# Performance work log

Hardware: AMD Instinct MI355X
Metric: run time of the kernel (lower is better)

## Reference

```python
import jax, jax.numpy as jnp
import numpy as np
import math

B, HW, EMBED, HEADS, WS = 32, 56, 192, 6, 7
SHIFT = WS // 2
HD = EMBED // HEADS
NW = HW // WS
NEG = -1e9  # stands in for -inf in the original; avoids NaN-safe issues while masking fully


def _shift_masks():
    # row_mask masks interaction between the cyclically-wrapped bottom strip and the rest
    k = WS * SHIFT
    row = np.zeros((WS * WS, WS * WS), np.float32)
    row[-k:, :-k] = NEG
    row[:-k, -k:] = NEG
    # column mask: rearrange '(r w1) (c w2) -> (w1 r) (w2 c)'
    col = row.reshape(WS, WS, WS, WS).transpose(1, 0, 3, 2).reshape(WS * WS, WS * WS)
    return jnp.asarray(row), jnp.asarray(col)


def setup_inputs() -> dict:
    key = jax.random.key(0)
    k = jax.random.split(key, 4)
    s = 1.0 / math.sqrt(EMBED)
    return {
        "x": jax.random.normal(k[0], (B, HW * HW, EMBED), jnp.float32),
        "w_qkv": jax.random.normal(k[1], (EMBED, 3 * EMBED), jnp.float32) * s,
        "b_qkv": jnp.zeros((3 * EMBED,), jnp.float32),
        "w_out": jax.random.normal(k[2], (EMBED, EMBED), jnp.float32) * s,
        "b_out": jnp.zeros((EMBED,), jnp.float32),
        "rel_bias": jax.random.normal(k[3], (WS * WS, WS * WS), jnp.float32) * 0.02,
    }


def reference(x, w_qkv, b_qkv, w_out, b_out, rel_bias):
    row_mask, col_mask = _shift_masks()
    qkv = x @ w_qkv + b_qkv                                  # [B, L, 3C]
    # original rearranges '(c K)' with K=3 -> K is the fastest-varying axis
    qkv = qkv.reshape(B, HW, HW, EMBED, 3)
    qkv = jnp.roll(qkv, (-SHIFT, -SHIFT), axis=(1, 2))       # cyclic shift
    # window partition: [B, heads, nh, nw, ws*ws, head_dim, 3]
    qkv = qkv.reshape(B, NW, WS, NW, WS, HEADS, HD, 3)
    qkv = qkv.transpose(0, 5, 1, 3, 2, 4, 6, 7).reshape(B, HEADS, NW, NW, WS * WS, HD, 3)
    q, k_, v = qkv[..., 0], qkv[..., 1], qkv[..., 2]
    scores = jnp.einsum('bhxymd,bhxynd->bhxymn', q, k_) / math.sqrt(HD)
    scores = scores + rel_bias                               # relative position bias [49,49]
    # shift masks only on the last window row / last window column
    scores = scores.at[:, :, -1, :].add(row_mask)
    scores = scores.at[:, :, :, -1].add(col_mask)
    attn = jax.nn.softmax(scores, axis=-1)
    out = jnp.einsum('bhxymn,bhxynd->bhxymd', attn, v)       # [B,H,nh,nw,49,hd]
    # merge windows back to the feature map
    out = out.reshape(B, HEADS, NW, NW, WS, WS, HD)
    out = out.transpose(0, 2, 4, 3, 5, 1, 6).reshape(B, HW, HW, EMBED)
    out = jnp.roll(out, (SHIFT, SHIFT), axis=(1, 2))         # reverse cyclic shift
    return out.reshape(B, HW * HW, EMBED) @ w_out + b_out
```

## Files before the change

kernel.cpp:

```cpp
#include <hip/hip_runtime.h>
#include <math.h>

typedef __bf16 bf16x8 __attribute__((ext_vector_type(8)));
typedef float f32x4 __attribute__((ext_vector_type(4)));
typedef unsigned short u16;

constexpr int Bn  = 32;
constexpr int HWn = 56;
constexpr int En  = 192;
constexpr int SH  = 3;
constexpr int NWn = 8;
constexpr int Ln  = HWn * HWn;
constexpr int Mn  = 49;
#define NEGV (-1e9f)

#define MFMA(a, b, c) __builtin_amdgcn_mfma_f32_16x16x32_bf16((a), (b), (c), 0, 0, 0)

__device__ __forceinline__ u16 f2b(float f) {
    unsigned u = __float_as_uint(f);
    return (u16)((u + 0x7fffu + ((u >> 16) & 1u)) >> 16);
}

__device__ __forceinline__ int xm384(int row) {
    return ((row & 3) << 4) | (((row >> 2) & 1) << 6);
}

__global__ __launch_bounds__(256) void prep_w(const float* __restrict__ wq,
                                              const float* __restrict__ wo,
                                              u16* __restrict__ wt,
                                              u16* __restrict__ wt2, int do2) {
    int i = blockIdx.x * 256 + threadIdx.x;
    if (i < 576 * 192) {
        int cp = i / 192, k = i - cp * 192;
        int comp = cp / 192, e = cp - comp * 192;
        wt[i] = f2b(wq[k * 576 + e * 3 + comp]);
    } else if (do2) {
        int i2 = i - 576 * 192;
        if (i2 < 192 * 192) {
            int c = i2 / 192, k = i2 - c * 192;
            wt2[i2] = f2b(wo[k * 192 + c]);
        }
    }
}

template<bool USE_WT, bool BF16OUT>
__global__ __launch_bounds__(512, 2) void swin_attn_mfma(
    const float* __restrict__ x, const u16* __restrict__ wt,
    const float* __restrict__ wq_f32, const float* __restrict__ b_qkv,
    const float* __restrict__ rel_bias, void* __restrict__ attn_outv)
{
    __shared__ char lds[73728] __attribute__((aligned(128)));

    const int tid  = threadIdx.x;
    const int w    = tid >> 6;
    const int lane = tid & 63;
    const int lq   = lane & 15;
    const int g    = lane >> 4;

    const int blk = blockIdx.x;
    const int wx = blk & 7, wy = (blk >> 3) & 7, b = blk >> 6;

    for (int j = tid; j < 64 * 48; j += 512) {
        int m = j / 48, q = j - 48 * m;
        u16 v[4];
        if (m < Mn) {
            int rr = m / 7, cc = m - 7 * rr;
            int oi = (wy * 7 + rr + SH) % HWn;
            int oj = (wx * 7 + cc + SH) % HWn;
            const float4 f = *(const float4*)(x + ((size_t)((b * HWn + oi) * HWn + oj)) * En + 4 * q);
            v[0] = f2b(f.x); v[1] = f2b(f.y); v[2] = f2b(f.z); v[3] = f2b(f.w);
        } else { v[0] = v[1] = v[2] = v[3] = 0; }
        *(ushort4*)(lds + m * 384 + ((8 * q) ^ xm384(m))) = *(ushort4*)v;
    }

    f32x4 acc[4][5];
    const f32x4 zero4 = {0.f, 0.f, 0.f, 0.f};
    #pragma unroll
    for (int mf = 0; mf < 4; mf++)
        #pragma unroll
        for (int j = 0; j < 5; j++) acc[mf][j] = zero4;

    bf16x8 wreg[5];
    auto stage = [&](int kt) {
        #pragma unroll
        for (int i2 = 0; i2 < 5; i2++) {
            int jj = tid + 512 * i2;
            if (jj < 2304) {
                int c = jj >> 2, q = jj & 3;
                if (USE_WT) {
                    wreg[i2] = *(const bf16x8*)(wt + c * 192 + kt * 32 + q * 8);
                } else {
                    int comp = c / 192, e = c - comp * 192;
                    int col = e * 3 + comp;
                    union { bf16x8 v; u16 a[8]; } t;
                    #pragma unroll
                    for (int p = 0; p < 8; p++)
                        t.a[p] = f2b(wq_f32[(size_t)(kt * 32 + q * 8 + p) * 576 + col]);
                    wreg[i2] = t.v;
                }
            }
        }
    };

    stage(0);
    __syncthreads();
    for (int kt = 0; kt < 6; kt++) {
        #pragma unroll
        for (int i2 = 0; i2 < 5; i2++) {
            int jj = tid + 512 * i2;
            if (jj < 2304) {
                int c = jj >> 2, q = jj & 3;
                *(bf16x8*)(lds + 24576 + c * 80 + 16 * q) = wreg[i2];
            }
        }
        __syncthreads();
        if (kt < 5) stage(kt + 1);

        bf16x8 af[4];
        #pragma unroll
        for (int mf = 0; mf < 4; mf++) {
            int m = 16 * mf + lq;
            af[mf] = *(const bf16x8*)(lds + m * 384 + ((64 * kt + 16 * g) ^ xm384(m)));
        }
        #pragma unroll
        for (int j = 0; j < 5; j++) {
            int nf = w + 8 * j;
            if (nf < 36) {
                int c = 16 * nf + lq;
                bf16x8 bfr = *(const bf16x8*)(lds + 24576 + c * 80 + 16 * g);
                #pragma unroll
                for (int mf = 0; mf < 4; mf++)
                    acc[mf][j] = MFMA(af[mf], bfr, acc[mf][j]);
            }
        }
        __syncthreads();
    }

    const float qscale = 0.17677669529663687f;
    #pragma unroll
    for (int j = 0; j < 5; j++) {
        int nf = w + 8 * j;
        if (nf >= 36) continue;
        int comp = nf / 12;
        int e = (nf - comp * 12) * 16 + lq;
        float bcol = b_qkv[e * 3 + comp];
        int h = e >> 5, d = e & 31;
        #pragma unroll
        for (int mf = 0; mf < 4; mf++) {
            #pragma unroll
            for (int r = 0; r < 4; r++) {
                int m = 16 * mf + 4 * g + r;
                float v = acc[mf][j][r] + bcol;
                int byte;
                if (comp == 0) { v *= qscale; byte = h * 4096 + m * 64 + ((2 * d) ^ (((m >> 1) & 3) << 4)); }
                else if (comp == 1) { byte = 24576 + h * 4096 + m * 64 + ((2 * d) ^ (((m >> 1) & 3) << 4)); }
                else { byte = 49152 + h * 4096 + d * 128 + ((2 * m) ^ ((d & 7) << 4)); }
                *(u16*)(lds + byte) = f2b(v);
            }
        }
    }
    __syncthreads();

    const int tb = w & 3, hg = w >> 2;
    const int t = 16 * tb + lq;
    bf16x8 qreg[3];
    #pragma unroll
    for (int hh = 0; hh < 3; hh++) {
        int h = hg * 3 + hh;
        int m = 16 * tb + lq;
        qreg[hh] = *(const bf16x8*)(lds + h * 4096 + m * 64 + ((16 * g) ^ (((m >> 1) & 3) << 4)));
    }
    const bool lastR = (wy == 7), lastC = (wx == 7);
    float bias[4][4];
    #pragma unroll
    for (int mi = 0; mi < 4; mi++)
        #pragma unroll
        for (int r = 0; r < 4; r++) {
            int key = 16 * mi + 4 * g + r;
            float bv;
            if (t < Mn) {
                if (key < Mn) {
                    bv = rel_bias[t * 49 + key];
                    if (lastR && ((t >= 28) != (key >= 28))) bv += NEGV;
                    if (lastC && ((t % 7 >= 4) != (key % 7 >= 4))) bv += NEGV;
                } else bv = NEGV;
            } else bv = 0.f;
            bias[mi][r] = bv;
        }
    size_t obase[4]; bool oval[4];
    #pragma unroll
    for (int r = 0; r < 4; r++) {
        int tok = 16 * tb + 4 * g + r;
        oval[r] = tok < Mn;
        int tk = oval[r] ? tok : 0;
        int rr = tk / 7, cc = tk - 7 * rr;
        int oi = (wy * 7 + rr + SH) % HWn;
        int oj = (wx * 7 + cc + SH) % HWn;
        obase[r] = ((size_t)((b * HWn + oi) * HWn + oj)) * En;
    }
    __syncthreads();

    #pragma unroll
    for (int hh = 0; hh < 3; hh++) {
        int h = hg * 3 + hh;
        f32x4 st[4];
        #pragma unroll
        for (int mi = 0; mi < 4; mi++) {
            int key = 16 * mi + lq;
            bf16x8 kf = *(const bf16x8*)(lds + 24576 + h * 4096 + key * 64 + ((16 * g) ^ (((key >> 1) & 3) << 4)));
            st[mi] = MFMA(kf, qreg[hh], zero4);
        }
        float mx = -3.4e38f;
        #pragma unroll
        for (int mi = 0; mi < 4; mi++)
            #pragma unroll
            for (int r = 0; r < 4; r++) {
                st[mi][r] += bias[mi][r];
                mx = fmaxf(mx, st[mi][r]);
            }
        mx = fmaxf(mx, __shfl_xor(mx, 16));
        mx = fmaxf(mx, __shfl_xor(mx, 32));
        float sum = 0.f;
        #pragma unroll
        for (int mi = 0; mi < 4; mi++)
            #pragma unroll
            for (int r = 0; r < 4; r++) {
                float e = __expf(st[mi][r] - mx);
                st[mi][r] = e; sum += e;
            }
        sum += __shfl_xor(sum, 16);
        sum += __shfl_xor(sum, 32);
        float inv = 1.f / sum;
        #pragma unroll
        for (int mi = 0; mi < 4; mi++)
            #pragma unroll
            for (int r = 0; r < 4; r++) {
                int key = 16 * mi + 4 * g + r;
                *(u16*)(lds + w * 2048 + lq * 128 + ((2 * key) ^ ((lq & 7) << 4))) = f2b(st[mi][r] * inv);
            }
        f32x4 o0 = zero4, o1 = zero4;
        #pragma unroll
        for (int kf2 = 0; kf2 < 2; kf2++) {
            bf16x8 pf = *(const bf16x8*)(lds + w * 2048 + lq * 128 + ((64 * kf2 + 16 * g) ^ ((lq & 7) << 4)));
            int d0 = lq, d1 = 16 + lq;
            bf16x8 v0 = *(const bf16x8*)(lds + 49152 + h * 4096 + d0 * 128 + ((64 * kf2 + 16 * g) ^ ((d0 & 7) << 4)));
            bf16x8 v1 = *(const bf16x8*)(lds + 49152 + h * 4096 + d1 * 128 + ((64 * kf2 + 16 * g) ^ ((d1 & 7) << 4)));
            o0 = MFMA(pf, v0, o0);
            o1 = MFMA(pf, v1, o1);
        }
        #pragma unroll
        for (int r = 0; r < 4; r++) {
            if (oval[r]) {
                if (BF16OUT) {
                    u16* ab = (u16*)attn_outv;
                    ab[obase[r] + h * 32 + lq]      = f2b(o0[r]);
                    ab[obase[r] + h * 32 + 16 + lq] = f2b(o1[r]);
                } else {
                    float* ab = (float*)attn_outv;
                    ab[obase[r] + h * 32 + lq]      = o0[r];
                    ab[obase[r] + h * 32 + 16 + lq] = o1[r];
                }
            }
        }
    }
}

template<bool BF16IN, bool USE_WT2>
__global__ __launch_bounds__(512) void swin_proj_mfma(
    const void* __restrict__ attn_in, const u16* __restrict__ wt2,
    const float* __restrict__ w_out, const float* __restrict__ b_out,
    float* __restrict__ out)
{
    __shared__ char lds[122880] __attribute__((aligned(128)));
    const int tid = threadIdx.x;
    const size_t tok0 = (size_t)blockIdx.x * 128;

    for (int j = tid; j < 192 * 24; j += 512) {
        int c = j / 24, q = j - 24 * c;
        bf16x8 v;
        if (USE_WT2) {
            v = *(const bf16x8*)(wt2 + c * 192 + 8 * q);
        } else {
            union { bf16x8 v; u16 a[8]; } t;
            #pragma unroll
            for (int p = 0; p < 8; p++)
                t.a[p] = f2b(w_out[(8 * q + p) * 192 + c]);
            v = t.v;
        }
        *(bf16x8*)(lds + 49152 + c * 384 + ((16 * q) ^ xm384(c))) = v;
    }
    for (int j = tid; j < 128 * 24; j += 512) {
        int m = j / 24, q = j - 24 * m;
        bf16x8 v;
        if (BF16IN) {
            v = *(const bf16x8*)((const u16*)attn_in + (tok0 + m) * En + 8 * q);
        } else {
            const float* src = (const float*)attn_in + (tok0 + m) * En + 8 * q;
            float4 f0 = *(const float4*)src, f1 = *(const float4*)(src + 4);
            union { bf16x8 v; u16 a[8]; } t;
            t.a[0] = f2b(f0.x); t.a[1] = f2b(f0.y); t.a[2] = f2b(f0.z); t.a[3] = f2b(f0.w);
            t.a[4] = f2b(f1.x); t.a[5] = f2b(f1.y); t.a[6] = f2b(f1.z); t.a[7] = f2b(f1.w);
            v = t.v;
        }
        *(bf16x8*)(lds + m * 384 + ((16 * q) ^ xm384(m))) = v;
    }
    __syncthreads();

    const int w  = tid >> 6;
    const int lq = tid & 15;
    const int g  = (tid & 63) >> 4;

    f32x4 acc[12];
    #pragma unroll
    for (int nf = 0; nf < 12; nf++) {
        float bj = b_out[16 * nf + lq];
        acc[nf] = (f32x4){bj, bj, bj, bj};
    }
    #pragma unroll
    for (int kt = 0; kt < 6; kt++) {
        int m = 16 * w + lq;
        bf16x8 af = *(const bf16x8*)(lds + m * 384 + ((64 * kt + 16 * g) ^ xm384(m)));
        #pragma unroll
        for (int nf = 0; nf < 12; nf++) {
            int c = 16 * nf + lq;
            bf16x8 bf = *(const bf16x8*)(lds + 49152 + c * 384 + ((64 * kt + 16 * g) ^ xm384(c)));
            acc[nf] = MFMA(af, bf, acc[nf]);
        }
    }
    #pragma unroll
    for (int nf = 0; nf < 12; nf++)
        #pragma unroll
        for (int r = 0; r < 4; r++)
            out[(tok0 + 16 * w + 4 * g + r) * En + 16 * nf + lq] = acc[nf][r];
}

extern "C" void kernel_launch(void* const* d_in, const int* in_sizes, int n_in,
                              void* d_out, int out_size, void* d_ws, size_t ws_size,
                              hipStream_t stream) {
    const float* x        = (const float*)d_in[0];
    const float* w_qkv    = (const float*)d_in[1];
    const float* b_qkv    = (const float*)d_in[2];
    const float* w_out    = (const float*)d_in[3];
    const float* b_out    = (const float*)d_in[4];
    const float* rel_bias = (const float*)d_in[5];
    float* out = (float*)d_out;

    const size_t WT  = 576 * 192 * 2;
    const size_t WT2 = 192 * 192 * 2;
    const size_t A2  = (size_t)Bn * Ln * En * 2;
    char* ws = (char*)d_ws;

    const int GRID_A = Bn * NWn * NWn;
    const int GRID_B = (Bn * Ln) / 128;

    if (ws_size >= WT + WT2 + A2) {
        u16* wt  = (u16*)ws;
        u16* wt2 = (u16*)(ws + WT);
        u16* attn2 = (u16*)(ws + WT + WT2);
        prep_w<<<576, 256, 0, stream>>>(w_qkv, w_out, wt, wt2, 1);
        swin_attn_mfma<true, true><<<GRID_A, 512, 0, stream>>>(x, wt, w_qkv, b_qkv, rel_bias, attn2);
        swin_proj_mfma<true, true><<<GRID_B, 512, 0, stream>>>(attn2, wt2, w_out, b_out, out);
    } else if (ws_size >= WT + WT2) {
        u16* wt  = (u16*)ws;
        u16* wt2 = (u16*)(ws + WT);
        prep_w<<<576, 256, 0, stream>>>(w_qkv, w_out, wt, wt2, 1);
        swin_attn_mfma<true, false><<<GRID_A, 512, 0, stream>>>(x, wt, w_qkv, b_qkv, rel_bias, out);
        swin_proj_mfma<false, true><<<GRID_B, 512, 0, stream>>>(out, wt2, w_out, b_out, out);
    } else if (ws_size >= WT) {
        u16* wt = (u16*)ws;
        prep_w<<<432, 256, 0, stream>>>(w_qkv, w_out, wt, nullptr, 0);
        swin_attn_mfma<true, false><<<GRID_A, 512, 0, stream>>>(x, wt, w_qkv, b_qkv, rel_bias, out);
        swin_proj_mfma<false, false><<<GRID_B, 512, 0, stream>>>(out, nullptr, w_out, b_out, out);
    } else {
        swin_attn_mfma<false, false><<<GRID_A, 512, 0, stream>>>(x, nullptr, w_qkv, b_qkv, rel_bias, out);
        swin_proj_mfma<false, false><<<GRID_B, 512, 0, stream>>>(out, nullptr, w_out, b_out, out);
    }
}
```

Measured before the change: 285.8 us.

## Fuse output projection into windowed attention kernel, dropping intermediate buffer

The attention kernel now keeps each window's per-head outputs in registers, writes them as bf16 into shared memory, and runs the 192x192 output projection inside the same block before scattering the final rows to their shifted positions. This removes the separate projection kernel launch and the round trip of the bf16 attention intermediate through global memory. In exchange, each window block reads the projection weights directly from global memory (L2) instead of staging them in LDS. It also holds more accumulator registers, which may put pressure on the two-blocks-per-CU occupancy target.

```diff
diff --git a/kernel.cpp b/kernel.cpp
--- a/kernel.cpp
+++ b/kernel.cpp
@@ -43,11 +43,13 @@
     }
 }
 
-template<bool USE_WT, bool BF16OUT>
-__global__ __launch_bounds__(512, 2) void swin_attn_mfma(
+template<bool USE_WT, bool USE_WT2>
+__global__ __launch_bounds__(512, 2) void swin_fused(
     const float* __restrict__ x, const u16* __restrict__ wt,
+    const u16* __restrict__ wt2,
     const float* __restrict__ wq_f32, const float* __restrict__ b_qkv,
-    const float* __restrict__ rel_bias, void* __restrict__ attn_outv)
+    const float* __restrict__ w_out, const float* __restrict__ b_out,
+    const float* __restrict__ rel_bias, float* __restrict__ out)
 {
     __shared__ char lds[73728] __attribute__((aligned(128)));
 
@@ -187,19 +189,9 @@
             } else bv = 0.f;
             bias[mi][r] = bv;
         }
-    size_t obase[4]; bool oval[4];
-    #pragma unroll
-    for (int r = 0; r < 4; r++) {
-        int tok = 16 * tb + 4 * g + r;
-        oval[r] = tok < Mn;
-        int tk = oval[r] ? tok : 0;
-        int rr = tk / 7, cc = tk - 7 * rr;
-        int oi = (wy * 7 + rr + SH) % HWn;
-        int oj = (wx * 7 + cc + SH) % HWn;
-        obase[r] = ((size_t)((b * HWn + oi) * HWn + oj)) * En;
-    }
-    __syncthreads();
-
+    __syncthreads();
+
+    f32x4 oacc[3][2];
     #pragma unroll
     for (int hh = 0; hh < 3; hh++) {
         int h = hg * 3 + hh;
@@ -248,90 +240,74 @@
             o0 = MFMA(pf, v0, o0);
             o1 = MFMA(pf, v1, o1);
         }
+        oacc[hh][0] = o0;
+        oacc[hh][1] = o1;
+    }
+
+    __syncthreads();
+    #pragma unroll
+    for (int hh = 0; hh < 3; hh++) {
+        int h = hg * 3 + hh;
         #pragma unroll
         for (int r = 0; r < 4; r++) {
-            if (oval[r]) {
-                if (BF16OUT) {
-                    u16* ab = (u16*)attn_outv;
-                    ab[obase[r] + h * 32 + lq]      = f2b(o0[r]);
-                    ab[obase[r] + h * 32 + 16 + lq] = f2b(o1[r]);
-                } else {
-                    float* ab = (float*)attn_outv;
-                    ab[obase[r] + h * 32 + lq]      = o0[r];
-                    ab[obase[r] + h * 32 + 16 + lq] = o1[r];
-                }
-            }
-        }
-    }
-}
-
-template<bool BF16IN, bool USE_WT2>
-__global__ __launch_bounds__(512) void swin_proj_mfma(
-    const void* __restrict__ attn_in, const u16* __restrict__ wt2,
-    const float* __restrict__ w_out, const float* __restrict__ b_out,
-    float* __restrict__ out)
-{
-    __shared__ char lds[122880] __attribute__((aligned(128)));
-    const int tid = threadIdx.x;
-    const size_t tok0 = (size_t)blockIdx.x * 128;
-
-    for (int j = tid; j < 192 * 24; j += 512) {
-        int c = j / 24, q = j - 24 * c;
-        bf16x8 v;
-        if (USE_WT2) {
-            v = *(const bf16x8*)(wt2 + c * 192 + 8 * q);
-        } else {
-            union { bf16x8 v; u16 a[8]; } t;
-            #pragma unroll
-            for (int p = 0; p < 8; p++)
-                t.a[p] = f2b(w_out[(8 * q + p) * 192 + c]);
-            v = t.v;
-        }
-        *(bf16x8*)(lds + 49152 + c * 384 + ((16 * q) ^ xm384(c))) = v;
-    }
-    for (int j = tid; j < 128 * 24; j += 512) {
-        int m = j / 24, q = j - 24 * m;
-        bf16x8 v;
-        if (BF16IN) {
-            v = *(const bf16x8*)((const u16*)attn_in + (tok0 + m) * En + 8 * q);
-        } else {
-            const float* src = (const float*)attn_in + (tok0 + m) * En + 8 * q;
-            float4 f0 = *(const float4*)src, f1 = *(const float4*)(src + 4);
-            union { bf16x8 v; u16 a[8]; } t;
-            t.a[0] = f2b(f0.x); t.a[1] = f2b(f0.y); t.a[2] = f2b(f0.z); t.a[3] = f2b(f0.w);
-            t.a[4] = f2b(f1.x); t.a[5] = f2b(f1.y); t.a[6] = f2b(f1.z); t.a[7] = f2b(f1.w);
-            v = t.v;
-        }
-        *(bf16x8*)(lds + m * 384 + ((16 * q) ^ xm384(m))) = v;
-    }
-    __syncthreads();
-
-    const int w  = tid >> 6;
-    const int lq = tid & 15;
-    const int g  = (tid & 63) >> 4;
-
-    f32x4 acc[12];
-    #pragma unroll
-    for (int nf = 0; nf < 12; nf++) {
-        float bj = b_out[16 * nf + lq];
-        acc[nf] = (f32x4){bj, bj, bj, bj};
-    }
+            int tk = 16 * tb + 4 * g + r;
+            int c0 = h * 32 + lq;
+            *(u16*)(lds + 24576 + tk * 384 + ((2 * c0) ^ xm384(tk)))        = f2b(oacc[hh][0][r]);
+            *(u16*)(lds + 24576 + tk * 384 + ((2 * (c0 + 16)) ^ xm384(tk))) = f2b(oacc[hh][1][r]);
+        }
+    }
+    __syncthreads();
+
+    const int wm = w >> 2, wn = w & 3;
+    f32x4 pacc[2][3];
+    #pragma unroll
+    for (int mi = 0; mi < 2; mi++)
+        #pragma unroll
+        for (int nj = 0; nj < 3; nj++) {
+            float bj = b_out[16 * (3 * wn + nj) + lq];
+            pacc[mi][nj] = (f32x4){bj, bj, bj, bj};
+        }
     #pragma unroll
     for (int kt = 0; kt < 6; kt++) {
-        int m = 16 * w + lq;
-        bf16x8 af = *(const bf16x8*)(lds + m * 384 + ((64 * kt + 16 * g) ^ xm384(m)));
-        #pragma unroll
-        for (int nf = 0; nf < 12; nf++) {
-            int c = 16 * nf + lq;
-            bf16x8 bf = *(const bf16x8*)(lds + 49152 + c * 384 + ((64 * kt + 16 * g) ^ xm384(c)));
-            acc[nf] = MFMA(af, bf, acc[nf]);
-        }
-    }
-    #pragma unroll
-    for (int nf = 0; nf < 12; nf++)
-        #pragma unroll
-        for (int r = 0; r < 4; r++)
-            out[(tok0 + 16 * w + 4 * g + r) * En + 16 * nf + lq] = acc[nf][r];
+        bf16x8 paf[2];
+        #pragma unroll
+        for (int mi = 0; mi < 2; mi++) {
+            int row = 16 * (2 * wm + mi) + lq;
+            paf[mi] = *(const bf16x8*)(lds + 24576 + row * 384 + ((64 * kt + 16 * g) ^ xm384(row)));
+        }
+        #pragma unroll
+        for (int nj = 0; nj < 3; nj++) {
+            int c = 16 * (3 * wn + nj) + lq;
+            bf16x8 pbf;
+            if (USE_WT2) {
+                pbf = *(const bf16x8*)(wt2 + c * 192 + kt * 32 + 8 * g);
+            } else {
+                union { bf16x8 v; u16 a[8]; } tt;
+                #pragma unroll
+                for (int p = 0; p < 8; p++)
+                    tt.a[p] = f2b(w_out[(kt * 32 + 8 * g + p) * 192 + c]);
+                pbf = tt.v;
+            }
+            #pragma unroll
+            for (int mi = 0; mi < 2; mi++)
+                pacc[mi][nj] = MFMA(paf[mi], pbf, pacc[mi][nj]);
+        }
+    }
+    #pragma unroll
+    for (int mi = 0; mi < 2; mi++)
+        #pragma unroll
+        for (int r = 0; r < 4; r++) {
+            int tok = 16 * (2 * wm + mi) + 4 * g + r;
+            if (tok < Mn) {
+                int rr = tok / 7, cc = tok - 7 * rr;
+                int oi = (wy * 7 + rr + SH) % HWn;
+                int oj = (wx * 7 + cc + SH) % HWn;
+                float* dst = out + ((size_t)((b * HWn + oi) * HWn + oj)) * En;
+                #pragma unroll
+                for (int nj = 0; nj < 3; nj++)
+                    dst[16 * (3 * wn + nj) + lq] = pacc[mi][nj][r];
+            }
+        }
 }
 
 extern "C" void kernel_launch(void* const* d_in, const int* in_sizes, int n_in,
@@ -347,32 +323,23 @@
 
     const size_t WT  = 576 * 192 * 2;
     const size_t WT2 = 192 * 192 * 2;
-    const size_t A2  = (size_t)Bn * Ln * En * 2;
     char* ws = (char*)d_ws;
 
     const int GRID_A = Bn * NWn * NWn;
-    const int GRID_B = (Bn * Ln) / 128;
-
-    if (ws_size >= WT + WT2 + A2) {
-        u16* wt  = (u16*)ws;
-        u16* wt2 = (u16*)(ws + WT);
-        u16* attn2 = (u16*)(ws + WT + WT2);
-        prep_w<<<576, 256, 0, stream>>>(w_qkv, w_out, wt, wt2, 1);
-        swin_attn_mfma<true, true><<<GRID_A, 512, 0, stream>>>(x, wt, w_qkv, b_qkv, rel_bias, attn2);
-        swin_proj_mfma<true, true><<<GRID_B, 512, 0, stream>>>(attn2, wt2, w_out, b_out, out);
-    } else if (ws_size >= WT + WT2) {
+
+    if (ws_size >= WT + WT2) {
         u16* wt  = (u16*)ws;
         u16* wt2 = (u16*)(ws + WT);
         prep_w<<<576, 256, 0, stream>>>(w_qkv, w_out, wt, wt2, 1);
-        swin_attn_mfma<true, false><<<GRID_A, 512, 0, stream>>>(x, wt, w_qkv, b_qkv, rel_bias, out);
-        swin_proj_mfma<false, true><<<GRID_B, 512, 0, stream>>>(out, wt2, w_out, b_out, out);
+        swin_fused<true, true><<<GRID_A, 512, 0, stream>>>(
+            x, wt, wt2, w_qkv, b_qkv, w_out, b_out, rel_bias, out);
     } else if (ws_size >= WT) {
         u16* wt = (u16*)ws;
         prep_w<<<432, 256, 0, stream>>>(w_qkv, w_out, wt, nullptr, 0);
-        swin_attn_mfma<true, false><<<GRID_A, 512, 0, stream>>>(x, wt, w_qkv, b_qkv, rel_bias, out);
-        swin_proj_mfma<false, false><<<GRID_B, 512, 0, stream>>>(out, nullptr, w_out, b_out, out);
+        swin_fused<true, false><<<GRID_A, 512, 0, stream>>>(
+            x, wt, nullptr, w_qkv, b_qkv, w_out, b_out, rel_bias, out);
     } else {
-        swin_attn_mfma<false, false><<<GRID_A, 512, 0, stream>>>(x, nullptr, w_qkv, b_qkv, rel_bias, out);
-        swin_proj_mfma<false, false><<<GRID_B, 512, 0, stream>>>(out, nullptr, w_out, b_out, out);
-    }
-}
+        swin_fused<false, false><<<GRID_A, 512, 0, stream>>>(
+            x, nullptr, nullptr, w_qkv, b_qkv, w_out, b_out, rel_bias, out);
+    }
+}
```

Result: no change. 283.3 us (-0.8%).
